# Kernel optimization log

Measured on AMD Instinct MI355X. Metric: run time of the kernel, lower is better.

The kernel has to match this reference:

```python
import jax, jax.numpy as jnp
import numpy as np

B0, K, H, W = 8, 1, 512, 512
S, CS, NMS, M = 25, 51, 5, 2048
REG_W, COV_POW = 1.0, 0.5

def _gauss_kernel(n):
    x = jnp.linspace(-1.0, 1.0, n)
    g = jnp.exp(-x * x / 0.5)
    return g / g.sum()

def _conv1d2d(x, k1d, horizontal, pad_h, pad_w):
    # x: [B,1,H,W]; replicates torch F.conv2d with the given (possibly asymmetric) padding
    kern = k1d.reshape(1, 1, 1, -1) if horizontal else k1d.reshape(1, 1, -1, 1)
    return jax.lax.conv_general_dilated(x, kern, (1, 1), [(pad_h, pad_h), (pad_w, pad_w)],
                                        dimension_numbers=("NCHW", "OIHW", "NCHW"))

def bilinear_sample(img, pts):
    # img [B,C,H,W], pts [B,N,2] (x,y in [-1,1]); grid_sample bilinear, align_corners=False, zero padding
    Bb, C, Hh, Ww = img.shape
    x = (pts[..., 0] + 1.0) * 0.5 * Ww - 0.5
    y = (pts[..., 1] + 1.0) * 0.5 * Hh - 0.5
    x0 = jnp.floor(x); y0 = jnp.floor(y)
    wx = x - x0; wy = y - y0
    x0i = x0.astype(jnp.int32); y0i = y0.astype(jnp.int32)
    flat = img.reshape(Bb, C, Hh * Ww)
    def tap(yi, xi, w):
        ok = ((yi >= 0) & (yi < Hh) & (xi >= 0) & (xi < Ww)).astype(img.dtype)
        idx = jnp.clip(yi, 0, Hh - 1) * Ww + jnp.clip(xi, 0, Ww - 1)  # [B,N]
        v = jnp.take_along_axis(flat, idx[:, None, :], axis=2)        # [B,C,N]
        return v * (w * ok)[:, None, :]
    return (tap(y0i, x0i, (1 - wy) * (1 - wx)) + tap(y0i, x0i + 1, (1 - wy) * wx)
            + tap(y0i + 1, x0i, wy * (1 - wx)) + tap(y0i + 1, x0i + 1, wy * wx))

def compute_matchability(keypoint_p, has_depth, Bt):
    G = _gauss_kernel(S)
    # NOTE: faithful to original asymmetric padding bug: pad H while convolving along W, then pad W while convolving along H
    s = _conv1d2d(keypoint_p.reshape(Bt, 1, H, W), G, True, S // 2, 0)
    s = _conv1d2d(s, G, False, 0, S // 2)
    log_p_hat = jax.nn.log_softmax(jnp.log(s.reshape(Bt, H * W) + 1e-8), axis=-1)
    sd = _conv1d2d(has_depth.reshape(Bt, 1, H, W), G, True, 0, S // 2)
    sd = _conv1d2d(sd, G, False, S // 2, 0).reshape(Bt, H * W)
    p = sd / sd.sum(-1, keepdims=True)
    return jnp.sum(jnp.where(p > 0, p * (jnp.log(jnp.maximum(p, 1e-30)) - log_p_hat), 0.0), axis=-1)

def sample_keypoints(sm):
    # sm [B,H,W]; coverage-reweighted NMS + top-k (topk=True, subpixel=False)
    wcov = jnp.exp(-jnp.square(jnp.linspace(-2.0, 2.0, CS)))
    ld = _conv1d2d(((sm + 1e-6) * 1e4)[:, None], wcov, True, 0, CS // 2)
    ld = _conv1d2d(ld, wcov, False, CS // 2, 0)[:, 0]
    sm = sm * (ld + 1e-8) ** (-COV_POW)
    p = NMS // 2
    mx = jax.lax.reduce_window(sm, -jnp.inf, jax.lax.max, (1, NMS, NMS), (1, 1, 1),
                               [(0, 0), (p, p), (p, p)])
    sm = sm * (sm == mx)
    _, inds = jax.lax.top_k(sm.reshape(-1, H * W), M)
    xs = (jnp.arange(W) + 0.5) * 2.0 / W - 1.0
    ys = (jnp.arange(H) + 0.5) * 2.0 / H - 1.0
    grid = jnp.stack(jnp.meshgrid(xs, ys, indexing="xy"), axis=-1).reshape(H * W, 2)
    return jnp.take(grid, inds, axis=0)  # [B,M,2] normalized (x,y)

def masked_log_softmax(logits, mask):
    return jax.nn.log_softmax(jnp.where(mask, logits, -1e9), axis=-1)

def _reward(d):
    return jnp.exp(-100.0 * d)

def _forward(scoremap, gt_warp_A2B, gt_warp_B2A, valid_A2B, valid_B2A, has_depth):
    sg = jax.lax.stop_gradient
    lA = scoremap[:B0].reshape(B0, K, H * W)
    lB = scoremap[B0:].reshape(B0, K, H * W)
    logits = jnp.concatenate([lA, lB], 0)                                   # [2B,K,HW]
    kp_p = jax.nn.softmax(logits.reshape(2 * B0, K * H * W), -1).reshape(2 * B0, K, H * W).sum(1)
    match_loss = compute_matchability(kp_p, sg(has_depth), 2 * B0).mean()
    # sparse branch is under torch.set_grad_enabled(False)
    kpts_A = sample_keypoints(sg(kp_p[:B0]).reshape(B0, H, W))
    kpts_B = sample_keypoints(sg(kp_p[B0:]).reshape(B0, H, W))
    kpts_A2B = bilinear_sample(sg(gt_warp_A2B[..., 2:]).transpose(0, 3, 1, 2), kpts_A).transpose(0, 2, 1)
    kpts_B2A = bilinear_sample(sg(gt_warp_B2A[..., 2:]).transpose(0, 3, 1, 2), kpts_B).transpose(0, 2, 1)
    legit_A2B = bilinear_sample(sg(valid_A2B)[:, None], kpts_A)[:, 0] > 0   # [B,M]
    legit_B2A = bilinear_sample(sg(valid_B2A)[:, None], kpts_B)[:, 0] > 0
    dA = jnp.sqrt(jnp.sum(jnp.square(kpts_A2B[:, :, None] - kpts_B[:, None]), -1) + 1e-12).min(-1)
    dB = jnp.sqrt(jnp.sum(jnp.square(kpts_B2A[:, :, None] - kpts_A[:, None]), -1) + 1e-12).min(-1)
    rA = _reward(dA); rB = _reward(dB)
    slA = bilinear_sample(lA.reshape(B0, 1, H, W), kpts_A)[:, 0]            # [B,M]
    slB = bilinear_sample(lB.reshape(B0, 1, H, W), kpts_B)[:, 0]
    lpA = masked_log_softmax(slA, legit_A2B)
    lpB = masked_log_softmax(slB, legit_B2A)
    sparse = -jnp.sum(jnp.where(legit_A2B, rA * lpA, 0.0)) - jnp.sum(jnp.where(legit_B2A, rB * lpB, 0.0))
    return sparse + REG_W * match_loss

def setup_inputs() -> dict:
    key = jax.random.key(0)
    ks = jax.random.split(key, 6)
    scoremap = jax.random.normal(ks[0], (2 * B0, K, H, W), jnp.float32)
    gt_warp_A2B = jax.random.uniform(ks[1], (B0, H, W, 4), jnp.float32, -1.0, 1.0)
    gt_warp_B2A = jax.random.uniform(ks[2], (B0, H, W, 4), jnp.float32, -1.0, 1.0)
    valid_A2B = (jax.random.uniform(ks[3], (B0, H, W)) > 0.3).astype(jnp.float32)
    valid_B2A = (jax.random.uniform(ks[4], (B0, H, W)) > 0.3).astype(jnp.float32)
    has_depth = (jax.random.uniform(ks[5], (2 * B0, H, W)) > 0.3).astype(jnp.float32)
    return dict(scoremap=scoremap, gt_warp_A2B=gt_warp_A2B, gt_warp_B2A=gt_warp_B2A,
                valid_A2B=valid_A2B, valid_B2A=valid_B2A, has_depth=has_depth)

def reference(scoremap, gt_warp_A2B, gt_warp_B2A, valid_A2B, valid_B2A, has_depth):
    return _forward(scoremap, gt_warp_A2B, gt_warp_B2A, valid_A2B, valid_B2A, has_depth)
```

## Files before the change

kernel.cpp:

```cpp
#include <hip/hip_runtime.h>

#define HH 512
#define WW 512
#define HW_ 262144
#define NIMG 16
#define MK 2048
#define CAPB 4096
#define SCAP 32768
#define SBUFN 768

static constexpr size_t OFF_B1    = 16777216;
static constexpr size_t OFF_B2    = 33554432;
static constexpr size_t OFF_SMALL = 50331648;
static constexpr size_t OFF_SEL  = 4194304;
static constexpr size_t OFF_BND  = 4325376;
static constexpr size_t OFF_PP   = 4849664;
static constexpr size_t OFF_WXp  = 5111808;
static constexpr size_t OFF_WYp  = 5242880;
static constexpr size_t OFF_LG   = 5373952;
static constexpr size_t OFF_SL   = 5505024;
static constexpr size_t OFF_PMIN = 5636096;
static constexpr size_t OFF_HIST = 33554432;
static constexpr size_t OFF_SURV = 33554432 + 4194304;

#define CSTRIDE 32

__device__ __forceinline__ float wred64(float v) {
  for (int m = 1; m < 64; m <<= 1) v += __shfl_xor(v, m);
  return v;
}

__device__ __forceinline__ void g25_wave0(float* g) {
  int t = threadIdx.x;
  if (t < 64) {
    float raw = 0.0f;
    if (t < 25) {
      float x = -1.0f + (float)t * (2.0f / 24.0f);
      raw = expf(-(x * x) / 0.5f);
    }
    float s = raw;
    for (int m = 1; m < 64; m <<= 1) s += __shfl_xor(s, m);
    if (t < 25) g[t] = raw / s;
  }
}
__device__ __forceinline__ void w51_wave0(float* wc) {
  int t = threadIdx.x;
  if (t < 51) {
    float x = -2.0f + (float)t * (4.0f / 50.0f);
    wc[t] = expf(-x * x);
  }
}

template<int B>
__device__ __forceinline__ float brsum(float v, float* red) {
  int t = threadIdx.x;
  red[t] = v; __syncthreads();
  for (int s = B >> 1; s > 0; s >>= 1) {
    if (t < s) red[t] += red[t + s];
    __syncthreads();
  }
  float r = red[0]; __syncthreads();
  return r;
}
template<int B>
__device__ __forceinline__ float brmax(float v, float* red) {
  int t = threadIdx.x;
  red[t] = v; __syncthreads();
  for (int s = B >> 1; s > 0; s >>= 1) {
    if (t < s) red[t] = fmaxf(red[t], red[t + s]);
    __syncthreads();
  }
  float r = red[0]; __syncthreads();
  return r;
}

__global__ void __launch_bounds__(256)
k_pre(const float* __restrict__ x, const float* __restrict__ hd, float* A,
      float* sume, float* sumS, float* Zb) {
  __shared__ float g[25];
  __shared__ float red[12];
  int tid = threadIdx.x;
  g25_wave0(g);
  size_t base = (size_t)blockIdx.x * 1024;
  size_t e = base + tid * 4;
  float4 xs = *(const float4*)(x + e);
  float4 hs = *(const float4*)(hd + e);
  __syncthreads();
  int rem = (int)(e & (HW_ - 1));
  int y = rem >> 9, x0 = rem & 511;
  float wv = 0.0f;
  {
    int k0 = y - 499; if (k0 < 0) k0 = 0;
    int k1 = y + 12;  if (k1 > 24) k1 = 24;
    for (int k = k0; k <= k1; k++) wv += g[k];
  }
  float cwv[4], cpv[4];
  {
    int lo = x0 - 487; if (lo < 0) lo = 0;
    int hi = x0;       if (hi > 24) hi = 24;
    float c = 0.0f;
    for (int d = lo; d <= hi; d++) c += g[d];
    cwv[0] = c;
    for (int q = 1; q < 4; q++) {
      int i = x0 + q;
      if (i <= 24) c += g[i];
      if (i >= 488) c -= g[i - 488];
      cwv[q] = c;
    }
  }
  {
    int lo = x0 - 499; if (lo < 0) lo = 0;
    int hi = x0 + 12;  if (hi > 24) hi = 24;
    float c = 0.0f;
    for (int d = lo; d <= hi; d++) c += g[d];
    cpv[0] = c;
    for (int q = 1; q < 4; q++) {
      int i = x0 + q;
      if (i + 12 <= 24) c += g[i + 12];
      if (i >= 500) c -= g[i - 500];
      cpv[q] = c;
    }
  }
  float e0 = expf(xs.x), e1 = expf(xs.y), e2 = expf(xs.z), e3 = expf(xs.w);
  *(float4*)(A + e) = make_float4(e0, e1, e2, e3);
  float r0 = (e0 + e1) + (e2 + e3);
  float r1 = (e0 * cwv[0] + e1 * cwv[1] + e2 * cwv[2] + e3 * cwv[3]) * wv;
  float r2 = (hs.x * cpv[0] + hs.y * cpv[1] + hs.z * cpv[2] + hs.w * cpv[3]) * wv;
  r0 = wred64(r0); r1 = wred64(r1); r2 = wred64(r2);
  int wid = tid >> 6;
  if ((tid & 63) == 0) { red[wid] = r0; red[4 + wid] = r1; red[8 + wid] = r2; }
  __syncthreads();
  if (tid == 0) {
    int img = (int)(base >> 18);
    atomicAdd(&sume[img * CSTRIDE], red[0] + red[1] + red[2] + red[3]);
    atomicAdd(&sumS[img * CSTRIDE], red[4] + red[5] + red[6] + red[7]);
    atomicAdd(&Zb[img * CSTRIDE], red[8] + red[9] + red[10] + red[11]);
  }
}

__global__ void __launch_bounds__(256)
k_hconv(const float* __restrict__ A, const float* __restrict__ hd,
        const float* __restrict__ sume, float* b1, float* b2) {
  __shared__ __align__(16) float ta[512];
  __shared__ __align__(16) float th[536];
  __shared__ float g[25];
  int tid = threadIdx.x;
  int blk = blockIdx.x;
  int img = blk >> 9;
  size_t rowoff = (size_t)blk * 512;
  g25_wave0(g);
  ((float2*)ta)[tid] = *(const float2*)(A + rowoff + tid * 2);
  ((float2*)(th + 12))[tid] = *(const float2*)(hd + rowoff + tid * 2);
  if (tid < 12) { th[tid] = 0.0f; th[524 + tid] = 0.0f; }
  __syncthreads();
  float inv = 1.0f / sume[img * CSTRIDE];
  int j = 2 * tid;
  float v1a = 0.0f, v1b = 0.0f;
  if (tid >= 6 && tid <= 249) {
    float w[26];
#pragma unroll
    for (int d = 0; d < 26; d++) w[d] = ta[j - 12 + d];
#pragma unroll
    for (int d = 0; d < 25; d++) {
      v1a = fmaf(g[d], w[d], v1a);
      v1b = fmaf(g[d], w[d + 1], v1b);
    }
  }
  float v2a = 0.0f, v2b = 0.0f;
  {
    float u[26];
#pragma unroll
    for (int d = 0; d < 26; d++) u[d] = th[j + d];
#pragma unroll
    for (int d = 0; d < 25; d++) {
      v2a = fmaf(g[d], u[d], v2a);
      v2b = fmaf(g[d], u[d + 1], v2b);
    }
  }
  ((float2*)b1)[blk * 256 + tid] = make_float2(v1a * inv, v1b * inv);
  ((float2*)b2)[blk * 256 + tid] = make_float2(v2a, v2b);
}

__global__ void __launch_bounds__(256)
k_match(const float* __restrict__ b1, const float* __restrict__ b2,
        const float* __restrict__ sume, const float* sumS, const float* Zb,
        float* macc) {
  __shared__ float g[25];
  __shared__ float t1[88 * 64];
  __shared__ float t2[88 * 64];
  __shared__ float red4[4];
  g25_wave0(g);
  int blk = blockIdx.x;
  int img = blk >> 6;
  int ty = (blk >> 3) & 7;
  int tx = blk & 7;
  int y0 = ty * 64, x0 = tx * 64;
  const float* base1 = b1 + (size_t)img * HW_;
  const float* base2 = b2 + (size_t)img * HW_;
  for (int i = threadIdx.x; i < 88 * 64; i += 256) {
    int r = i >> 6, c = i & 63;
    int y = y0 + r - 12;
    float v1 = 0.0f, v2 = 0.0f;
    if (y >= 0 && y < 512) {
      size_t o = (size_t)y * 512 + x0 + c;
      v1 = base1[o]; v2 = base2[o];
    }
    t1[i] = v1; t2[i] = v2;
  }
  __syncthreads();
  float Z = Zb[img * CSTRIDE];
  float inv = 1.0f / sume[img * CSTRIDE];
  float logS = logf(sumS[img * CSTRIDE] * inv + (float)HW_ * 1e-8f);
  float acc = 0.0f;
  for (int w = threadIdx.x; w < 1024; w += 256) {
    int rg = w >> 6, c = w & 63;
    int r0 = rg * 4;
    float s[4] = {0.f, 0.f, 0.f, 0.f};
    float d[4] = {0.f, 0.f, 0.f, 0.f};
#pragma unroll
    for (int i = 0; i < 28; i++) {
      float v1 = t1[(r0 + i) * 64 + c];
      float v2 = t2[(r0 + i) * 64 + c];
#pragma unroll
      for (int jj = 0; jj < 4; jj++) {
        if (i >= jj && i - jj < 25) {
          s[jj] = fmaf(g[i - jj], v1, s[jj]);
          d[jj] = fmaf(g[i - jj], v2, d[jj]);
        }
      }
    }
#pragma unroll
    for (int jj = 0; jj < 4; jj++) {
      float p = d[jj] / Z;
      if (p > 0.0f)
        acc += p * (logf(fmaxf(p, 1e-30f)) - (logf(s[jj] + 1e-8f) - logS));
    }
  }
  acc = wred64(acc);
  if ((threadIdx.x & 63) == 0) red4[threadIdx.x >> 6] = acc;
  __syncthreads();
  if (threadIdx.x == 0)
    atomicAdd(macc, red4[0] + red4[1] + red4[2] + red4[3]);
}

__global__ void __launch_bounds__(256)
k_h51(const float* __restrict__ A, const float* __restrict__ sume, float* out) {
  __shared__ float wc[51];
  __shared__ __align__(16) float ta[564];
  int tid = threadIdx.x;
  int blk = blockIdx.x;
  int img = blk >> 9;
  size_t rowoff = (size_t)blk * 512;
  w51_wave0(wc);
  float s1 = 1e4f / sume[img * CSTRIDE];
  for (int i = tid; i < 562; i += 256) {
    int j = i - 25;
    ta[i] = ((unsigned)j < 512u) ? fmaf(A[rowoff + j], s1, 1e-2f) : 0.0f;
  }
  __syncthreads();
  int j = 2 * tid;
  float w[52];
#pragma unroll
  for (int d = 0; d < 52; d++) w[d] = ta[j + d];
  float va = 0.0f, vb = 0.0f;
#pragma unroll
  for (int d = 0; d < 51; d++) {
    va = fmaf(wc[d], w[d], va);
    vb = fmaf(wc[d], w[d + 1], vb);
  }
  ((float2*)out)[blk * 256 + tid] = make_float2(va, vb);
}

__global__ void __launch_bounds__(512)
k_smwnms(const float* __restrict__ A, const float* __restrict__ sume,
         const float* __restrict__ b1,
         unsigned long long* surv, unsigned* scnt, unsigned* hist) {
  __shared__ float wc[51];
  __shared__ float tb1[118 * 68];
  __shared__ float tsm[68 * 68];
  __shared__ unsigned long long sbuf[SBUFN];
  __shared__ unsigned lcnt;
  __shared__ unsigned gbase;
  float* hm = tb1;
  int tid = threadIdx.x;
  w51_wave0(wc);
  if (tid == 0) lcnt = 0;
  int blk = blockIdx.x;
  int img = blk >> 6;
  int ty = (blk >> 3) & 7;
  int tx = blk & 7;
  int y0 = ty * 64, x0 = tx * 64;
  const float* base = b1 + (size_t)img * HW_;
  for (int i = tid; i < 118 * 68; i += 512) {
    int r = i / 68, c = i - r * 68;
    int y = y0 + r - 27, x = x0 + c - 2;
    tb1[i] = (y >= 0 && y < 512 && x >= 0 && x < 512)
                 ? base[(size_t)y * 512 + x] : 0.0f;
  }
  __syncthreads();
  float inv = 1.0f / sume[img * CSTRIDE];
  const float* abase = A + (size_t)img * HW_;
  for (int w = tid; w < 68 * 17; w += 512) {
    int rg = w / 68, c = w - rg * 68;
    int r0 = rg * 4;
    float a[4] = {0.f, 0.f, 0.f, 0.f};
#pragma unroll
    for (int i = 0; i < 54; i++) {
      float v = tb1[(r0 + i) * 68 + c];
#pragma unroll
      for (int jj = 0; jj < 4; jj++) {
        if (i >= jj && i - jj < 51) a[jj] = fmaf(wc[i - jj], v, a[jj]);
      }
    }
#pragma unroll
    for (int jj = 0; jj < 4; jj++) {
      int r = r0 + jj;
      int y = y0 + r - 2, x = x0 + c - 2;
      float res = -3.4e38f;
      if (y >= 0 && y < 512 && x >= 0 && x < 512)
        res = (abase[(size_t)y * 512 + x] * inv) / sqrtf(a[jj] + 1e-8f);
      tsm[r * 68 + c] = res;
    }
  }
  __syncthreads();
  for (int i = tid; i < 68 * 64; i += 512) {
    int r = i >> 6, c = i & 63;
    const float* row = tsm + r * 68 + c;
    float m = fmaxf(fmaxf(row[0], row[1]), fmaxf(row[2], fmaxf(row[3], row[4])));
    hm[i] = m;
  }
  __syncthreads();
  for (int k0 = 0; k0 < 8; k0++) {
    int i = tid + k0 * 512;
    int r = i >> 6, c = i & 63;
    float v = tsm[(r + 2) * 68 + (c + 2)];
    float M = hm[r * 64 + c];
    M = fmaxf(M, hm[(r + 1) * 64 + c]);
    M = fmaxf(M, hm[(r + 2) * 64 + c]);
    M = fmaxf(M, hm[(r + 3) * 64 + c]);
    M = fmaxf(M, hm[(r + 4) * 64 + c]);
    bool keep = (v == M) && (v != 0.0f);
    if (keep) {
      unsigned p = atomicAdd(&lcnt, 1u);
      unsigned bits = __float_as_uint(v);
      unsigned idx = (unsigned)((y0 + r) * 512 + x0 + c);
      if (p < SBUFN)
        sbuf[p] = ((unsigned long long)bits << 32) |
                  (unsigned long long)(idx ^ 0xFFFFFFFFu);
      atomicAdd(&hist[(size_t)img * 65536 + (bits >> 16)], 1u);
    }
  }
  __syncthreads();
  unsigned total = lcnt; if (total > SBUFN) total = SBUFN;
  if (tid == 0) gbase = atomicAdd(&scnt[img * CSTRIDE], total);
  __syncthreads();
  unsigned gb = gbase;
  for (unsigned i = tid; i < total; i += 512) {
    unsigned p = gb + i;
    if (p < SCAP) surv[(size_t)img * SCAP + p] = sbuf[i];
  }
}

__global__ void k_thresh(const unsigned* __restrict__ hist, unsigned* Tb, unsigned* needb) {
  int img = blockIdx.x;
  const unsigned* h = hist + (size_t)img * 65536;
  __shared__ unsigned part[256];
  __shared__ unsigned scan[257];
  int t = threadIdx.x;
  unsigned s = 0;
  for (int k = 0; k < 256; k++) {
    int bin = 65535 - (t * 256 + k);
    s += (bin == 0) ? 0x00100000u : h[bin];
  }
  part[t] = s; __syncthreads();
  if (t == 0) {
    unsigned c = 0;
    for (int k = 0; k < 256; k++) { scan[k] = c; c += part[k]; }
    scan[256] = c;
  }
  __syncthreads();
  unsigned pre = scan[t];
  if (pre < MK && pre + part[t] >= MK) {
    unsigned c = pre;
    for (int k = 0; k < 256; k++) {
      int bin = 65535 - (t * 256 + k);
      unsigned cnt = (bin == 0) ? 0x00100000u : h[bin];
      if (c + cnt >= MK) { Tb[img * CSTRIDE] = (unsigned)bin; needb[img * CSTRIDE] = MK - c; break; }
      c += cnt;
    }
  }
}

__global__ void k_collect(const unsigned long long* __restrict__ surv,
                          const unsigned* __restrict__ scnt,
                          const unsigned* __restrict__ Tb,
                          unsigned* selcnt, unsigned* sel,
                          unsigned* bcnt, unsigned long long* bnd) {
  int blk = blockIdx.x;
  int img = blk >> 7;
  int i = (blk & 127) * 256 + threadIdx.x;
  unsigned cnt = scnt[img * CSTRIDE]; if (cnt > SCAP) cnt = SCAP;
  unsigned long long entry = ((unsigned)i < cnt) ? surv[(size_t)img * SCAP + i] : 0ull;
  unsigned bits = (unsigned)(entry >> 32);
  unsigned bin = bits >> 16;
  unsigned T = Tb[img * CSTRIDE];
  bool ok = (unsigned)i < cnt;
  bool c1 = ok && (bin > T);
  bool c2 = ok && (bin == T);
  int lane = threadIdx.x & 63;
  unsigned long long lowmask = (1ull << lane) - 1ull;

  unsigned long long m1 = __ballot(c1);
  if (m1) {
    int leader = __ffsll(m1) - 1;
    unsigned base = 0;
    if (lane == leader) base = atomicAdd(&selcnt[img * CSTRIDE], (unsigned)__popcll(m1));
    base = __shfl(base, leader);
    if (c1) {
      unsigned p = base + (unsigned)__popcll(m1 & lowmask);
      if (p < MK) sel[img * MK + p] = (unsigned)(entry & 0xFFFFFFFFull) ^ 0xFFFFFFFFu;
    }
  }
  unsigned long long m2 = __ballot(c2);
  if (m2) {
    int leader = __ffsll(m2) - 1;
    unsigned base = 0;
    if (lane == leader) base = atomicAdd(&bcnt[img * CSTRIDE], (unsigned)__popcll(m2));
    base = __shfl(base, leader);
    if (c2) {
      unsigned p = base + (unsigned)__popcll(m2 & lowmask);
      if (p < CAPB) bnd[(size_t)img * CAPB + p] = entry;
    }
  }
}

__global__ void __launch_bounds__(1024)
k_finsel(const unsigned long long* __restrict__ bnd, const unsigned* bcnt,
         const unsigned* needb, const unsigned* selcnt, unsigned* sel) {
  int img = blockIdx.x;
  __shared__ unsigned long long key[CAPB];
  unsigned bn = bcnt[img * CSTRIDE];
  int n = (bn < CAPB) ? (int)bn : CAPB;
  int np2 = 2;
  while (np2 < n) np2 <<= 1;
  int t = threadIdx.x;
  for (int k = t; k < np2; k += 1024)
    key[k] = (k < n) ? bnd[(size_t)img * CAPB + k] : 0ull;
  __syncthreads();
  for (int sz = 2; sz <= np2; sz <<= 1) {
    for (int st = sz >> 1; st > 0; st >>= 1) {
      for (int i = t; i < np2; i += 1024) {
        int l = i ^ st;
        if (l > i) {
          unsigned long long a = key[i], b = key[l];
          bool up = ((i & sz) == 0);
          if (up ? (a < b) : (a > b)) { key[i] = b; key[l] = a; }
        }
      }
      __syncthreads();
    }
  }
  unsigned c1 = selcnt[img * CSTRIDE]; if (c1 > MK) c1 = MK;
  unsigned need = needb[img * CSTRIDE];
  unsigned kk = need; if (kk > MK - c1) kk = MK - c1;
  for (unsigned m = t; m < MK - c1; m += 1024) {
    unsigned v = 0u;
    if (m < kk && m < (unsigned)n)
      v = (unsigned)(key[m] & 0xFFFFFFFFull) ^ 0xFFFFFFFFu;
    sel[img * MK + c1 + m] = v;
  }
}

__global__ void k_prep(const unsigned* __restrict__ sel, const float* __restrict__ scoremap,
                       const float* __restrict__ gtA, const float* __restrict__ gtB,
                       const float* __restrict__ vA, const float* __restrict__ vB,
                       float2* pp, float* wx, float* wy, float* lg, float* sl) {
  int t = blockIdx.x * 256 + threadIdx.x;
  int img = t >> 11;
  unsigned idx = sel[t] & (HW_ - 1);
  int h = idx >> 9, w = idx & 511;
  pp[t] = make_float2((w + 0.5f) * (2.0f / 512.0f) - 1.0f,
                      (h + 0.5f) * (2.0f / 512.0f) - 1.0f);
  int b = (img < 8) ? img : img - 8;
  const float* gt = (img < 8) ? gtA : gtB;
  const float* vv = (img < 8) ? vA : vB;
  size_t pix = (size_t)b * HW_ + idx;
  float2 gxy = *(const float2*)(gt + pix * 4 + 2);
  wx[t] = gxy.x;
  wy[t] = gxy.y;
  lg[t] = (vv[pix] > 0.0f) ? 1.0f : 0.0f;
  sl[t] = scoremap[(size_t)img * HW_ + idx];
}

__global__ void __launch_bounds__(256)
k_mindist(const float2* __restrict__ pp,
          const float* __restrict__ wx, const float* __restrict__ wy,
          float* pmin) {
  __shared__ float2 opp[512];
  int blk = blockIdx.x;
  int img = blk >> 5;
  int qc = (blk >> 2) & 7;
  int oc = blk & 3;
  const float2* ob = pp + (size_t)(img ^ 8) * MK + oc * 512;
  for (int k = threadIdx.x; k < 512; k += 256) opp[k] = ob[k];
  __syncthreads();
  int m = img * MK + qc * 256 + threadIdx.x;
  float ax = wx[m], ay = wy[m];
  float d[8];
#pragma unroll
  for (int u = 0; u < 8; u++) d[u] = 3.4e38f;
  for (int n = 0; n < 512; n += 8) {
#pragma unroll
    for (int u = 0; u < 8; u++) {
      float2 o = opp[n + u];
      float dx = ax - o.x, dy = ay - o.y;
      d[u] = fminf(d[u], fmaf(dx, dx, dy * dy));
    }
  }
  float d2 = fminf(fminf(fminf(d[0], d[1]), fminf(d[2], d[3])),
                   fminf(fminf(d[4], d[5]), fminf(d[6], d[7])));
  pmin[oc * (NIMG * MK) + m] = d2;
}

__global__ void __launch_bounds__(1024)
k_loss(const float* __restrict__ sl, const float* __restrict__ lg,
       const float* __restrict__ pmin, float* sacc) {
  int img = blockIdx.x;
  __shared__ float red[1024];
  int t = threadIdx.x;
  int i0 = img * MK + t, i1 = i0 + 1024;
  float s0 = sl[i0], s1 = sl[i1];
  float g0 = lg[i0], g1 = lg[i1];
  float l0 = (g0 > 0.0f) ? s0 : -1e9f;
  float l1 = (g1 > 0.0f) ? s1 : -1e9f;
  float mx = brmax<1024>(fmaxf(l0, l1), red);
  float se = brsum<1024>(expf(l0 - mx) + expf(l1 - mx), red);
  float lse = mx + logf(se);
  const int ST = NIMG * MK;
  float a = 0.0f;
  if (g0 > 0.0f) {
    float mn = fminf(fminf(pmin[i0], pmin[ST + i0]),
                     fminf(pmin[2 * ST + i0], pmin[3 * ST + i0]));
    float r0 = expf(-100.0f * sqrtf(mn + 1e-12f));
    a += r0 * (s0 - lse);
  }
  if (g1 > 0.0f) {
    float mn = fminf(fminf(pmin[i1], pmin[ST + i1]),
                     fminf(pmin[2 * ST + i1], pmin[3 * ST + i1]));
    float r1 = expf(-100.0f * sqrtf(mn + 1e-12f));
    a += r1 * (s1 - lse);
  }
  float tot = brsum<1024>(a, red);
  if (t == 0) atomicAdd(sacc, -tot);
}

__global__ void k_out(const float* macc, const float* sacc, float* out) {
  out[0] = sacc[0] + macc[0] * (1.0f / 16.0f);
}

extern "C" void kernel_launch(void* const* d_in, const int* in_sizes, int n_in,
                              void* d_out, int out_size, void* d_ws, size_t ws_size,
                              hipStream_t stream) {
  const float* scoremap = (const float*)d_in[0];
  const float* gtA = (const float*)d_in[1];
  const float* gtB = (const float*)d_in[2];
  const float* vA  = (const float*)d_in[3];
  const float* vB  = (const float*)d_in[4];
  const float* hd  = (const float*)d_in[5];

  char* ws = (char*)d_ws;
  float* A  = (float*)(ws);
  float* B1 = (float*)(ws + OFF_B1);

  char* sm = ws + OFF_SMALL;
  float*    sume   = (float*)(sm + 0);
  float*    sumS   = (float*)(sm + 2048);
  float*    Zb     = (float*)(sm + 4096);
  unsigned* Tb     = (unsigned*)(sm + 6144);
  unsigned* needb  = (unsigned*)(sm + 8192);
  unsigned* selcnt = (unsigned*)(sm + 10240);
  unsigned* bcnt   = (unsigned*)(sm + 12288);
  float*    macc   = (float*)(sm + 14336);
  float*    sacc   = (float*)(sm + 14464);
  unsigned* scnt   = (unsigned*)(sm + 16384);

  unsigned* hist = (unsigned*)(ws + OFF_HIST);
  unsigned long long* surv = (unsigned long long*)(ws + OFF_SURV);
  unsigned* sel  = (unsigned*)(ws + OFF_SEL);
  unsigned long long* bnd = (unsigned long long*)(ws + OFF_BND);
  float2* pp = (float2*)(ws + OFF_PP);
  float* wx = (float*)(ws + OFF_WXp);
  float* wy = (float*)(ws + OFF_WYp);
  float* lg = (float*)(ws + OFF_LG);
  float* sl = (float*)(ws + OFF_SL);
  float* pmin = (float*)(ws + OFF_PMIN);
  float* B2 = (float*)(ws + 33554432);

  float* out = (float*)d_out;

  hipMemsetAsync(sm, 0, 32768, stream);

  k_pre<<<4096, 256, 0, stream>>>(scoremap, hd, A, sume, sumS, Zb);

  k_hconv<<<8192, 256, 0, stream>>>(A, hd, sume, B1, B2);
  k_match<<<1024, 256, 0, stream>>>(B1, B2, sume, sumS, Zb, macc);

  k_h51<<<8192, 256, 0, stream>>>(A, sume, B1);
  hipMemsetAsync(ws + OFF_HIST, 0, (size_t)16 * 65536 * 4, stream);

  k_smwnms<<<1024, 512, 0, stream>>>(A, sume, B1, surv, scnt, hist);
  k_thresh<<<16, 256, 0, stream>>>(hist, Tb, needb);
  k_collect<<<2048, 256, 0, stream>>>(surv, scnt, Tb, selcnt, sel, bcnt, bnd);
  k_finsel<<<16, 1024, 0, stream>>>(bnd, bcnt, needb, selcnt, sel);

  k_prep<<<128, 256, 0, stream>>>(sel, scoremap, gtA, gtB, vA, vB, pp, wx, wy, lg, sl);
  k_mindist<<<512, 256, 0, stream>>>(pp, wx, wy, pmin);
  k_loss<<<16, 1024, 0, stream>>>(sl, lg, pmin, sacc);
  k_out<<<1, 1, 0, stream>>>(macc, sacc, out);
}
```

Baseline: 327.4 us.

## Fuse 51-tap horizontal conv into hconv and merge top-k selection kernels

Folds the 51-tap horizontal blur into k_hconv, which now writes it to a separate B3 buffer when the workspace is large enough. The affine scale and offset are applied after convolution, using analytic edge weight sums. This avoids a second full read of A and one kernel launch. It also merges threshold, collect and final-sort into a single per-image k_select kernel using shared-memory counters, and widens k_match blocks to 512 threads. The trade-offs are extra register pressure in hconv and only 16 blocks doing the collect scan.

```diff
diff --git a/kernel.cpp b/kernel.cpp
--- a/kernel.cpp
+++ b/kernel.cpp
@@ -12,8 +12,8 @@
 static constexpr size_t OFF_B1    = 16777216;
 static constexpr size_t OFF_B2    = 33554432;
 static constexpr size_t OFF_SMALL = 50331648;
+static constexpr size_t OFF_B3    = 51380224;
 static constexpr size_t OFF_SEL  = 4194304;
-static constexpr size_t OFF_BND  = 4325376;
 static constexpr size_t OFF_PP   = 4849664;
 static constexpr size_t OFF_WXp  = 5111808;
 static constexpr size_t OFF_WYp  = 5242880;
@@ -45,9 +45,16 @@
 }
 __device__ __forceinline__ void w51_wave0(float* wc) {
   int t = threadIdx.x;
-  if (t < 51) {
-    float x = -2.0f + (float)t * (4.0f / 50.0f);
-    wc[t] = expf(-x * x);
+  if (t < 64) {
+    float raw = 0.0f;
+    if (t < 51) {
+      float x = -2.0f + (float)t * (4.0f / 50.0f);
+      raw = expf(-x * x);
+    }
+    float s = raw;
+    for (int m = 1; m < 64; m <<= 1) s += __shfl_xor(s, m);
+    if (t < 51) wc[t] = raw;
+    if (t == 0) wc[51] = s;
   }
 }
 
@@ -140,30 +147,36 @@
 
 __global__ void __launch_bounds__(256)
 k_hconv(const float* __restrict__ A, const float* __restrict__ hd,
-        const float* __restrict__ sume, float* b1, float* b2) {
-  __shared__ __align__(16) float ta[512];
+        const float* __restrict__ sume, float* b1, float* b2, float* b3) {
+  __shared__ float ta[562];
   __shared__ __align__(16) float th[536];
   __shared__ float g[25];
+  __shared__ float wc[52];
   int tid = threadIdx.x;
   int blk = blockIdx.x;
   int img = blk >> 9;
   size_t rowoff = (size_t)blk * 512;
   g25_wave0(g);
-  ((float2*)ta)[tid] = *(const float2*)(A + rowoff + tid * 2);
+  w51_wave0(wc);
+  for (int i = tid; i < 562; i += 256) {
+    int j = i - 25;
+    ta[i] = ((unsigned)j < 512u) ? A[rowoff + j] : 0.0f;
+  }
   ((float2*)(th + 12))[tid] = *(const float2*)(hd + rowoff + tid * 2);
   if (tid < 12) { th[tid] = 0.0f; th[524 + tid] = 0.0f; }
   __syncthreads();
   float inv = 1.0f / sume[img * CSTRIDE];
+  float s1 = 1e4f * inv;
   int j = 2 * tid;
+  float w[52];
+#pragma unroll
+  for (int d = 0; d < 52; d++) w[d] = ta[j + d];
   float v1a = 0.0f, v1b = 0.0f;
   if (tid >= 6 && tid <= 249) {
-    float w[26];
-#pragma unroll
-    for (int d = 0; d < 26; d++) w[d] = ta[j - 12 + d];
 #pragma unroll
     for (int d = 0; d < 25; d++) {
-      v1a = fmaf(g[d], w[d], v1a);
-      v1b = fmaf(g[d], w[d + 1], v1b);
+      v1a = fmaf(g[d], w[13 + d], v1a);
+      v1b = fmaf(g[d], w[14 + d], v1b);
     }
   }
   float v2a = 0.0f, v2b = 0.0f;
@@ -179,16 +192,48 @@
   }
   ((float2*)b1)[blk * 256 + tid] = make_float2(v1a * inv, v1b * inv);
   ((float2*)b2)[blk * 256 + tid] = make_float2(v2a, v2b);
-}
-
-__global__ void __launch_bounds__(256)
+  if (b3) {
+    float va = 0.0f, vb = 0.0f;
+#pragma unroll
+    for (int d = 0; d < 51; d++) {
+      va = fmaf(wc[d], w[d], va);
+      vb = fmaf(wc[d], w[d + 1], vb);
+    }
+    float Wall = wc[51];
+    float Wra, Wrb;
+    {
+      int x = j;
+      if (x >= 25 && x <= 486) Wra = Wall;
+      else {
+        float r = 0.0f;
+        int lo = 25 - x; if (lo < 0) lo = 0;
+        int hi = 536 - x; if (hi > 50) hi = 50;
+        for (int d = lo; d <= hi; d++) r += wc[d];
+        Wra = r;
+      }
+      x = j + 1;
+      if (x >= 25 && x <= 486) Wrb = Wall;
+      else {
+        float r = 0.0f;
+        int lo = 25 - x; if (lo < 0) lo = 0;
+        int hi = 536 - x; if (hi > 50) hi = 50;
+        for (int d = lo; d <= hi; d++) r += wc[d];
+        Wrb = r;
+      }
+    }
+    ((float2*)b3)[blk * 256 + tid] =
+        make_float2(fmaf(va, s1, 1e-2f * Wra), fmaf(vb, s1, 1e-2f * Wrb));
+  }
+}
+
+__global__ void __launch_bounds__(512)
 k_match(const float* __restrict__ b1, const float* __restrict__ b2,
         const float* __restrict__ sume, const float* sumS, const float* Zb,
         float* macc) {
   __shared__ float g[25];
   __shared__ float t1[88 * 64];
   __shared__ float t2[88 * 64];
-  __shared__ float red4[4];
+  __shared__ float red8[8];
   g25_wave0(g);
   int blk = blockIdx.x;
   int img = blk >> 6;
@@ -197,7 +242,7 @@
   int y0 = ty * 64, x0 = tx * 64;
   const float* base1 = b1 + (size_t)img * HW_;
   const float* base2 = b2 + (size_t)img * HW_;
-  for (int i = threadIdx.x; i < 88 * 64; i += 256) {
+  for (int i = threadIdx.x; i < 88 * 64; i += 512) {
     int r = i >> 6, c = i & 63;
     int y = y0 + r - 12;
     float v1 = 0.0f, v2 = 0.0f;
@@ -212,7 +257,7 @@
   float inv = 1.0f / sume[img * CSTRIDE];
   float logS = logf(sumS[img * CSTRIDE] * inv + (float)HW_ * 1e-8f);
   float acc = 0.0f;
-  for (int w = threadIdx.x; w < 1024; w += 256) {
+  for (int w = threadIdx.x; w < 1024; w += 512) {
     int rg = w >> 6, c = w & 63;
     int r0 = rg * 4;
     float s[4] = {0.f, 0.f, 0.f, 0.f};
@@ -237,15 +282,18 @@
     }
   }
   acc = wred64(acc);
-  if ((threadIdx.x & 63) == 0) red4[threadIdx.x >> 6] = acc;
-  __syncthreads();
-  if (threadIdx.x == 0)
-    atomicAdd(macc, red4[0] + red4[1] + red4[2] + red4[3]);
+  if ((threadIdx.x & 63) == 0) red8[threadIdx.x >> 6] = acc;
+  __syncthreads();
+  if (threadIdx.x == 0) {
+    float tt = 0.0f;
+    for (int k = 0; k < 8; k++) tt += red8[k];
+    atomicAdd(macc, tt);
+  }
 }
 
 __global__ void __launch_bounds__(256)
 k_h51(const float* __restrict__ A, const float* __restrict__ sume, float* out) {
-  __shared__ float wc[51];
+  __shared__ float wc[52];
   __shared__ __align__(16) float ta[564];
   int tid = threadIdx.x;
   int blk = blockIdx.x;
@@ -275,7 +323,7 @@
 k_smwnms(const float* __restrict__ A, const float* __restrict__ sume,
          const float* __restrict__ b1,
          unsigned long long* surv, unsigned* scnt, unsigned* hist) {
-  __shared__ float wc[51];
+  __shared__ float wc[52];
   __shared__ float tb1[118 * 68];
   __shared__ float tsm[68 * 68];
   __shared__ unsigned long long sbuf[SBUFN];
@@ -361,91 +409,85 @@
   }
 }
 
-__global__ void k_thresh(const unsigned* __restrict__ hist, unsigned* Tb, unsigned* needb) {
+__global__ void __launch_bounds__(1024)
+k_select(const unsigned* __restrict__ hist,
+         const unsigned long long* __restrict__ surv,
+         const unsigned* __restrict__ scnt, unsigned* sel) {
   int img = blockIdx.x;
   const unsigned* h = hist + (size_t)img * 65536;
-  __shared__ unsigned part[256];
-  __shared__ unsigned scan[257];
+  __shared__ unsigned wtot[16];
+  __shared__ unsigned Tsh, needsh;
+  __shared__ unsigned c1sh, bcl;
+  __shared__ unsigned long long key[CAPB];
   int t = threadIdx.x;
+  int lane = t & 63, wid = t >> 6;
+  unsigned long long lowmask = (1ull << lane) - 1ull;
   unsigned s = 0;
-  for (int k = 0; k < 256; k++) {
-    int bin = 65535 - (t * 256 + k);
+  for (int k = 0; k < 64; k++) {
+    int bin = 65535 - (t * 64 + k);
     s += (bin == 0) ? 0x00100000u : h[bin];
   }
-  part[t] = s; __syncthreads();
+  unsigned v = s;
+  for (int m = 1; m < 64; m <<= 1) {
+    unsigned u = __shfl_up(v, m);
+    if (lane >= m) v += u;
+  }
+  if (lane == 63) wtot[wid] = v;
+  if (t == 0) { c1sh = 0; bcl = 0; }
+  __syncthreads();
   if (t == 0) {
     unsigned c = 0;
-    for (int k = 0; k < 256; k++) { scan[k] = c; c += part[k]; }
-    scan[256] = c;
-  }
-  __syncthreads();
-  unsigned pre = scan[t];
-  if (pre < MK && pre + part[t] >= MK) {
+    for (int w = 0; w < 16; w++) { unsigned x = wtot[w]; wtot[w] = c; c += x; }
+  }
+  __syncthreads();
+  unsigned pre = v - s + wtot[wid];
+  if (pre < MK && pre + s >= MK) {
     unsigned c = pre;
-    for (int k = 0; k < 256; k++) {
-      int bin = 65535 - (t * 256 + k);
+    for (int k = 0; k < 64; k++) {
+      int bin = 65535 - (t * 64 + k);
       unsigned cnt = (bin == 0) ? 0x00100000u : h[bin];
-      if (c + cnt >= MK) { Tb[img * CSTRIDE] = (unsigned)bin; needb[img * CSTRIDE] = MK - c; break; }
+      if (c + cnt >= MK) { Tsh = (unsigned)bin; needsh = MK - c; break; }
       c += cnt;
     }
   }
-}
-
-__global__ void k_collect(const unsigned long long* __restrict__ surv,
-                          const unsigned* __restrict__ scnt,
-                          const unsigned* __restrict__ Tb,
-                          unsigned* selcnt, unsigned* sel,
-                          unsigned* bcnt, unsigned long long* bnd) {
-  int blk = blockIdx.x;
-  int img = blk >> 7;
-  int i = (blk & 127) * 256 + threadIdx.x;
+  __syncthreads();
+  unsigned T = Tsh, need = needsh;
   unsigned cnt = scnt[img * CSTRIDE]; if (cnt > SCAP) cnt = SCAP;
-  unsigned long long entry = ((unsigned)i < cnt) ? surv[(size_t)img * SCAP + i] : 0ull;
-  unsigned bits = (unsigned)(entry >> 32);
-  unsigned bin = bits >> 16;
-  unsigned T = Tb[img * CSTRIDE];
-  bool ok = (unsigned)i < cnt;
-  bool c1 = ok && (bin > T);
-  bool c2 = ok && (bin == T);
-  int lane = threadIdx.x & 63;
-  unsigned long long lowmask = (1ull << lane) - 1ull;
-
-  unsigned long long m1 = __ballot(c1);
-  if (m1) {
-    int leader = __ffsll(m1) - 1;
-    unsigned base = 0;
-    if (lane == leader) base = atomicAdd(&selcnt[img * CSTRIDE], (unsigned)__popcll(m1));
-    base = __shfl(base, leader);
-    if (c1) {
-      unsigned p = base + (unsigned)__popcll(m1 & lowmask);
-      if (p < MK) sel[img * MK + p] = (unsigned)(entry & 0xFFFFFFFFull) ^ 0xFFFFFFFFu;
-    }
-  }
-  unsigned long long m2 = __ballot(c2);
-  if (m2) {
-    int leader = __ffsll(m2) - 1;
-    unsigned base = 0;
-    if (lane == leader) base = atomicAdd(&bcnt[img * CSTRIDE], (unsigned)__popcll(m2));
-    base = __shfl(base, leader);
-    if (c2) {
-      unsigned p = base + (unsigned)__popcll(m2 & lowmask);
-      if (p < CAPB) bnd[(size_t)img * CAPB + p] = entry;
-    }
-  }
-}
-
-__global__ void __launch_bounds__(1024)
-k_finsel(const unsigned long long* __restrict__ bnd, const unsigned* bcnt,
-         const unsigned* needb, const unsigned* selcnt, unsigned* sel) {
-  int img = blockIdx.x;
-  __shared__ unsigned long long key[CAPB];
-  unsigned bn = bcnt[img * CSTRIDE];
-  int n = (bn < CAPB) ? (int)bn : CAPB;
+  for (unsigned base = 0; base < cnt; base += 1024) {
+    unsigned i = base + t;
+    bool ok = i < cnt;
+    unsigned long long entry = ok ? surv[(size_t)img * SCAP + i] : 0ull;
+    unsigned bin = ((unsigned)(entry >> 32)) >> 16;
+    bool cA = ok && (bin > T);
+    bool cB = ok && (bin == T);
+    unsigned long long mA = __ballot(cA);
+    if (mA) {
+      int leader = __ffsll(mA) - 1;
+      unsigned bp = 0;
+      if (lane == leader) bp = atomicAdd(&c1sh, (unsigned)__popcll(mA));
+      bp = __shfl(bp, leader);
+      if (cA) {
+        unsigned p = bp + (unsigned)__popcll(mA & lowmask);
+        if (p < MK) sel[img * MK + p] = (unsigned)(entry & 0xFFFFFFFFull) ^ 0xFFFFFFFFu;
+      }
+    }
+    unsigned long long mB = __ballot(cB);
+    if (mB) {
+      int leader = __ffsll(mB) - 1;
+      unsigned bp = 0;
+      if (lane == leader) bp = atomicAdd(&bcl, (unsigned)__popcll(mB));
+      bp = __shfl(bp, leader);
+      if (cB) {
+        unsigned p = bp + (unsigned)__popcll(mB & lowmask);
+        if (p < CAPB) key[p] = entry;
+      }
+    }
+  }
+  __syncthreads();
+  int n = (int)bcl; if (n > CAPB) n = CAPB;
   int np2 = 2;
   while (np2 < n) np2 <<= 1;
-  int t = threadIdx.x;
-  for (int k = t; k < np2; k += 1024)
-    key[k] = (k < n) ? bnd[(size_t)img * CAPB + k] : 0ull;
+  for (int k = n + t; k < np2; k += 1024) key[k] = 0ull;
   __syncthreads();
   for (int sz = 2; sz <= np2; sz <<= 1) {
     for (int st = sz >> 1; st > 0; st >>= 1) {
@@ -460,14 +502,13 @@
       __syncthreads();
     }
   }
-  unsigned c1 = selcnt[img * CSTRIDE]; if (c1 > MK) c1 = MK;
-  unsigned need = needb[img * CSTRIDE];
+  unsigned c1 = c1sh; if (c1 > MK) c1 = MK;
   unsigned kk = need; if (kk > MK - c1) kk = MK - c1;
   for (unsigned m = t; m < MK - c1; m += 1024) {
-    unsigned v = 0u;
+    unsigned vv = 0u;
     if (m < kk && m < (unsigned)n)
-      v = (unsigned)(key[m] & 0xFFFFFFFFull) ^ 0xFFFFFFFFu;
-    sel[img * MK + c1 + m] = v;
+      vv = (unsigned)(key[m] & 0xFFFFFFFFull) ^ 0xFFFFFFFFu;
+    sel[img * MK + c1 + m] = vv;
   }
 }
 
@@ -571,15 +612,12 @@
   char* ws = (char*)d_ws;
   float* A  = (float*)(ws);
   float* B1 = (float*)(ws + OFF_B1);
+  float* B2 = (float*)(ws + OFF_B2);
 
   char* sm = ws + OFF_SMALL;
   float*    sume   = (float*)(sm + 0);
   float*    sumS   = (float*)(sm + 2048);
   float*    Zb     = (float*)(sm + 4096);
-  unsigned* Tb     = (unsigned*)(sm + 6144);
-  unsigned* needb  = (unsigned*)(sm + 8192);
-  unsigned* selcnt = (unsigned*)(sm + 10240);
-  unsigned* bcnt   = (unsigned*)(sm + 12288);
   float*    macc   = (float*)(sm + 14336);
   float*    sacc   = (float*)(sm + 14464);
   unsigned* scnt   = (unsigned*)(sm + 16384);
@@ -587,14 +625,16 @@
   unsigned* hist = (unsigned*)(ws + OFF_HIST);
   unsigned long long* surv = (unsigned long long*)(ws + OFF_SURV);
   unsigned* sel  = (unsigned*)(ws + OFF_SEL);
-  unsigned long long* bnd = (unsigned long long*)(ws + OFF_BND);
   float2* pp = (float2*)(ws + OFF_PP);
   float* wx = (float*)(ws + OFF_WXp);
   float* wy = (float*)(ws + OFF_WYp);
   float* lg = (float*)(ws + OFF_LG);
   float* sl = (float*)(ws + OFF_SL);
   float* pmin = (float*)(ws + OFF_PMIN);
-  float* B2 = (float*)(ws + 33554432);
+
+  bool big = ws_size >= OFF_B3 + (size_t)16777216;
+  float* B3 = big ? (float*)(ws + OFF_B3) : nullptr;
+  float* B51 = big ? B3 : B1;
 
   float* out = (float*)d_out;
 
@@ -602,16 +642,14 @@
 
   k_pre<<<4096, 256, 0, stream>>>(scoremap, hd, A, sume, sumS, Zb);
 
-  k_hconv<<<8192, 256, 0, stream>>>(A, hd, sume, B1, B2);
-  k_match<<<1024, 256, 0, stream>>>(B1, B2, sume, sumS, Zb, macc);
-
-  k_h51<<<8192, 256, 0, stream>>>(A, sume, B1);
+  k_hconv<<<8192, 256, 0, stream>>>(A, hd, sume, B1, B2, B3);
+  k_match<<<1024, 512, 0, stream>>>(B1, B2, sume, sumS, Zb, macc);
+
+  if (!big) k_h51<<<8192, 256, 0, stream>>>(A, sume, B1);
   hipMemsetAsync(ws + OFF_HIST, 0, (size_t)16 * 65536 * 4, stream);
 
-  k_smwnms<<<1024, 512, 0, stream>>>(A, sume, B1, surv, scnt, hist);
-  k_thresh<<<16, 256, 0, stream>>>(hist, Tb, needb);
-  k_collect<<<2048, 256, 0, stream>>>(surv, scnt, Tb, selcnt, sel, bcnt, bnd);
-  k_finsel<<<16, 1024, 0, stream>>>(bnd, bcnt, needb, selcnt, sel);
+  k_smwnms<<<1024, 512, 0, stream>>>(A, sume, B51, surv, scnt, hist);
+  k_select<<<16, 1024, 0, stream>>>(hist, surv, scnt, sel);
 
   k_prep<<<128, 256, 0, stream>>>(sel, scoremap, gtA, gtB, vA, vB, pp, wx, wy, lg, sl);
   k_mindist<<<512, 256, 0, stream>>>(pp, wx, wy, pmin);
```

Measured after the change: 389.3 us. 18.9% more time.
